# Performance work log

Measured on AMD Instinct MI355X. Metric: run time of the kernel, lower is better.

## Reference

```python
import jax, jax.numpy as jnp
import numpy as np

IGNORE_IDX = -100
DELTA_V = 0.5
DELTA_D = 1.5
PARAM_VAR = 1.0
PARAM_DIST = 1.0
PARAM_REG = 0.001
LOSS_WEIGHT = 1.0
K = 64  # static upper bound on number of instances (matches fill_max of instance_labels)


def setup_inputs() -> dict:
    key = jax.random.key(0)
    k1, k2, k3 = jax.random.split(key, 3)
    B, D, N = 8, 32, 131072
    embedding_logits = jax.random.normal(k1, (B, D, N), dtype=jnp.float32)
    semantic_labels = jax.random.randint(k2, (B, N), 0, 21, dtype=jnp.int64)
    instance_labels = jax.random.randint(k3, (B, N), 0, K, dtype=jnp.int64)
    return {
        "embedding_logits": embedding_logits,
        "semantic_labels": semantic_labels,
        "instance_labels": instance_labels,
        "feature_dim": D,
    }


def _single(x, cls, inst):
    # x: [N, D] embeddings, cls/inst: [N] int labels
    dtype = x.dtype
    valid = cls != IGNORE_IDX
    # points of class 1 are merged into instance 0 (intent of the torch code)
    inst = jnp.where(cls == 1, 0, inst)
    ids = jnp.where(valid, inst, K)  # invalid points -> extra bin K

    counts = jax.ops.segment_sum(valid.astype(dtype), ids, num_segments=K + 1)[:K]
    seg_sum = jax.ops.segment_sum(
        jnp.where(valid[:, None], x, jnp.zeros((), dtype)), ids, num_segments=K + 1
    )[:K]                                            # [K, D]
    mu = seg_sum / (counts[:, None] + 1e-8)          # [K, D] cluster means
    present = counts > 0                             # [K]
    n_inst = jnp.maximum(jnp.sum(present.astype(dtype)), 1.0)

    # intra-cluster variance term (L1 distance to own cluster mean, hinged)
    mu_pt = mu[jnp.clip(ids, 0, K - 1)]              # [N, D]
    d = jnp.sum(jnp.abs(x - mu_pt), axis=1)          # [N]
    d = jnp.square(jnp.maximum(d - DELTA_V, 0.0)) * valid.astype(dtype)
    l_var_seg = jax.ops.segment_sum(d, ids, num_segments=K + 1)[:K] / (counts + 1e-8)
    l_var = jnp.sum(l_var_seg) / n_inst

    # inter-cluster distance term over distinct present cluster pairs
    pdist = jnp.sum(jnp.abs(mu[:, None, :] - mu[None, :, :]), axis=-1)  # [K, K]
    pair_mask = present[:, None] & present[None, :] & ~jnp.eye(K, dtype=bool)
    hinge = jnp.square(jnp.maximum(2.0 * DELTA_D - pdist, 0.0)) * pair_mask.astype(dtype)
    npairs = jnp.sum(pair_mask.astype(dtype))
    l_dist = jnp.where(npairs > 0, jnp.sum(hinge) / jnp.maximum(npairs, 1.0), 0.0)

    # regularization: mean L1 norm of present cluster means
    l_reg = jnp.sum(jnp.sum(jnp.abs(mu), axis=1) * present.astype(dtype)) / n_inst

    l_var = PARAM_VAR * l_var
    l_dist = PARAM_DIST * l_dist
    l_reg = PARAM_REG * l_reg
    loss = LOSS_WEIGHT * (l_var + l_dist + l_reg)
    return loss, l_var, l_dist, l_reg


def reference(embedding_logits, semantic_labels, instance_labels, feature_dim):
    # embedding_logits: [B, D, N] -> per-point embeddings [B, N, D]
    x = jnp.transpose(embedding_logits, (0, 2, 1))
    loss, l_var, l_dist, l_reg = jax.vmap(_single)(x, semantic_labels, instance_labels)
    return (
        jnp.mean(loss),
        jnp.mean(l_var),
        jnp.mean(l_dist),
        jnp.mean(l_reg),
    )
```

## Files before the change

### kernel.cpp

```cpp
#include <hip/hip_runtime.h>


typedef unsigned char uchar;
typedef __attribute__((ext_vector_type(8)))  short bf16x8;
typedef __attribute__((ext_vector_type(16))) float f32x16;

#define IGNORE_IDX (-100)

constexpr int B = 8;
constexpr int D = 32;
constexpr int K = 64;
constexpr int NPTS = 131072;
constexpr int BPB  = 128;
constexpr int SPAN = 1024;
constexpr float DELTA_V = 0.5f;
constexpr float TWO_DELTA_D = 3.0f;
constexpr float PARAM_REG = 0.001f;

constexpr size_t OFF_MU  = (size_t)B * BPB * 2048;
constexpr size_t OFF_VP  = OFF_MU + (size_t)B * 2048;
constexpr size_t OFF_CNT = OFF_VP + (size_t)B * BPB * K;
constexpr size_t OFF_ID  = OFF_CNT + (size_t)B * K;

__device__ inline unsigned bfpack(unsigned a0, unsigned a1) {
    return __builtin_amdgcn_perm(a1, a0, 0x07060302u);
}

__global__ __launch_bounds__(256) void k0_ids(
    const int* __restrict__ sem, const int* __restrict__ inst,
    uchar* __restrict__ id8, int* __restrict__ cnt)
{
    __shared__ int s_cnt[K];
    const int t = threadIdx.x;
    const int b = blockIdx.x / (NPTS / 2048);
    if (t < K) s_cnt[t] = 0;
    __syncthreads();

    const int base = blockIdx.x * 2048 + t * 8;
    const int4 c0 = *(const int4*)(sem + base);
    const int4 c1 = *(const int4*)(sem + base + 4);
    const int4 i0 = *(const int4*)(inst + base);
    const int4 i1 = *(const int4*)(inst + base + 4);
    const int cl[8] = {c0.x, c0.y, c0.z, c0.w, c1.x, c1.y, c1.z, c1.w};
    const int il[8] = {i0.x, i0.y, i0.z, i0.w, i1.x, i1.y, i1.z, i1.w};

    unsigned w0 = 0, w1 = 0;
#pragma unroll
    for (int j = 0; j < 8; ++j) {
        const bool v = (cl[j] != IGNORE_IDX);
        int q = (cl[j] == 1) ? 0 : il[j];
        q = (q < 0) ? 0 : (q > K - 1 ? K - 1 : q);
        if (v) atomicAdd(&s_cnt[q], 1);
        const unsigned byte = v ? (unsigned)q : 255u;
        if (j < 4) w0 |= byte << (8 * j);
        else       w1 |= byte << (8 * (j - 4));
    }
    *(uint2*)(id8 + base) = make_uint2(w0, w1);
    __syncthreads();

    if (t < K) {
        const int c = s_cnt[t];
        if (c) atomicAdd(&cnt[b * K + t], c);
    }
}

__global__ __launch_bounds__(256) void k1_mfma(
    const float* __restrict__ x, const uchar* __restrict__ id8,
    float* __restrict__ part)
{
    __shared__ float s_part[4][2048];
    const int t = threadIdx.x, w = t >> 6, L = t & 63;
    const int g = L >> 5, ln = L & 31;
    const unsigned lnu = (unsigned)ln, lnp32 = (unsigned)(ln + 32);
    const int blk = blockIdx.x, b = blk >> 7, sp = blk & (BPB - 1);

    const unsigned* xrow = (const unsigned*)(x + (size_t)b * D * NPTS
                                             + (size_t)ln * NPTS + sp * SPAN);
    const uchar* idb = id8 + (size_t)b * NPTS + sp * SPAN;

    f32x16 acc0, acc1;
#pragma unroll
    for (int i = 0; i < 16; ++i) { acc0[i] = 0.f; acc1[i] = 0.f; }

    for (int it = 0; it < SPAN / 64; ++it) {
        const int n0 = (it * 4 + w) * 16 + g * 8;
        const uint2 idq = *(const uint2*)(idb + n0);
        const uint4 xa = *(const uint4*)(xrow + n0);
        const uint4 xc = *(const uint4*)(xrow + n0 + 4);

        union { unsigned u[4]; bf16x8 v; } Ah, B0, B1;
        Ah.u[0] = bfpack(xa.x + 0x8000u, xa.y + 0x8000u);
        Ah.u[1] = bfpack(xa.z + 0x8000u, xa.w + 0x8000u);
        Ah.u[2] = bfpack(xc.x + 0x8000u, xc.y + 0x8000u);
        Ah.u[3] = bfpack(xc.z + 0x8000u, xc.w + 0x8000u);
#pragma unroll
        for (int p = 0; p < 4; ++p) {
            const unsigned pair = ((p < 2) ? idq.x : idq.y) >> ((p & 1) * 16);
            const unsigned e0 = pair & 255u, e1 = (pair >> 8) & 255u;
            unsigned r0 = (e0 == lnu)   ? 0x3F80u : 0u;
            unsigned r1 = (e0 == lnp32) ? 0x3F80u : 0u;
            if (e1 == lnu)   r0 |= 0x3F800000u;
            if (e1 == lnp32) r1 |= 0x3F800000u;
            B0.u[p] = r0; B1.u[p] = r1;
        }
        acc0 = __builtin_amdgcn_mfma_f32_32x32x16_bf16(Ah.v, B0.v, acc0, 0, 0, 0);
        acc1 = __builtin_amdgcn_mfma_f32_32x32x16_bf16(Ah.v, B1.v, acc1, 0, 0, 0);
    }

#pragma unroll
    for (int r = 0; r < 16; ++r) {
        const int row = (r & 3) + 8 * (r >> 2) + 4 * g;
        s_part[w][row * 64 + ln]      = acc0[r];
        s_part[w][row * 64 + ln + 32] = acc1[r];
    }
    __syncthreads();

    float* dst = part + (size_t)blk * 2048;
    for (int i = t; i < 2048; i += 256)
        dst[i] = s_part[0][i] + s_part[1][i] + s_part[2][i] + s_part[3][i];
}

__global__ __launch_bounds__(256) void k2_mu(const float* __restrict__ part,
                                             const int* __restrict__ cnt,
                                             float* __restrict__ mu)
{
    const int gid  = blockIdx.x * 256 + threadIdx.x;
    const int b    = gid >> 11;
    const int cell = gid & 2047;
    const int k    = cell & 63;
    float s = 0.f;
    for (int blk = 0; blk < BPB; ++blk)
        s += part[((size_t)(b * BPB + blk) << 11) + cell];
    mu[(size_t)b * 2048 + cell] = s / ((float)cnt[b * K + k] + 1e-8f);
}

__global__ __launch_bounds__(256) void k3_mfma(
    const float* __restrict__ x, const uchar* __restrict__ id8,
    const float* __restrict__ mu, float* __restrict__ vpart)
{
    __shared__ float s_var[K];
    const int t = threadIdx.x, w = t >> 6, L = t & 63;
    const int g = L >> 5, ln = L & 31;
    const int blk = blockIdx.x, b = blk >> 7, sp = blk & (BPB - 1);
    if (t < K) s_var[t] = 0.f;

    union { unsigned u[4]; bf16x8 v; } MAh[4];
    const unsigned* mrow = (const unsigned*)(mu + (size_t)b * 2048 + ln * 64);
#pragma unroll
    for (int c = 0; c < 4; ++c) {
        const uint4 m0 = *(const uint4*)(mrow + c * 16 + g * 8);
        const uint4 m1 = *(const uint4*)(mrow + c * 16 + g * 8 + 4);
        MAh[c].u[0] = bfpack(m0.x + 0x8000u, m0.y + 0x8000u);
        MAh[c].u[1] = bfpack(m0.z + 0x8000u, m0.w + 0x8000u);
        MAh[c].u[2] = bfpack(m1.x + 0x8000u, m1.y + 0x8000u);
        MAh[c].u[3] = bfpack(m1.z + 0x8000u, m1.w + 0x8000u);
    }
    __syncthreads();

    const float* xb  = x + (size_t)b * D * NPTS + sp * SPAN;
    const uchar* idb = id8 + (size_t)b * NPTS + sp * SPAN;

    for (int it = 0; it < SPAN / 128; ++it) {
        const int n0 = (it * 4 + w) * 32;
        const unsigned myid = idb[n0 + ln];
        const unsigned m8 = (myid < 64u && (((myid >> 3) & 1u) == (unsigned)g))
                          ? (1u << (myid & 7u)) : 0u;
        unsigned dw[4];
#pragma unroll
        for (int p = 0; p < 4; ++p) {
            const unsigned b0 = (m8 >> (2 * p)) & 1u;
            const unsigned b1 = (m8 >> (2 * p + 1)) & 1u;
            dw[p] = (b0 | (b1 << 16)) * 0x3F80u;
        }
        const unsigned cstar = myid >> 4;
        f32x16 acc;
#pragma unroll
        for (int i = 0; i < 16; ++i) acc[i] = 0.f;
#pragma unroll
        for (int c = 0; c < 4; ++c) {
            union { unsigned u[4]; bf16x8 v; } Bc;
#pragma unroll
            for (int p = 0; p < 4; ++p) Bc.u[p] = (cstar == (unsigned)c) ? dw[p] : 0u;
            acc = __builtin_amdgcn_mfma_f32_32x32x16_bf16(MAh[c].v, Bc.v, acc, 0, 0, 0);
        }
        float s = 0.f;
#pragma unroll
        for (int r = 0; r < 16; ++r) {
            const int row = (r & 3) + 8 * (r >> 2) + 4 * g;
            s += fabsf(xb[(size_t)row * NPTS + n0 + ln] - acc[r]);
        }
        s += __shfl_xor(s, 32, 64);
        if (g == 0 && myid < 64u) {
            const float h = fmaxf(s - DELTA_V, 0.f);
            if (h > 0.f) unsafeAtomicAdd(&s_var[myid], h * h);
        }
    }
    __syncthreads();
    if (t < K) vpart[(size_t)blk * K + t] = s_var[t];
}

__device__ float block_reduce_sum512(float v, float* s_buf) {
    for (int o = 32; o > 0; o >>= 1) v += __shfl_down(v, o, 64);
    const int wid  = threadIdx.x >> 6;
    const int lane = threadIdx.x & 63;
    if (lane == 0) s_buf[wid] = v;
    __syncthreads();
    float r = 0.f;
    if (threadIdx.x == 0)
        for (int w = 0; w < 8; ++w) r += s_buf[w];
    __syncthreads();
    return r;
}

__global__ __launch_bounds__(512) void k4_final(const float* __restrict__ mu,
                                                const int* __restrict__ cnt,
                                                const float* __restrict__ vpart,
                                                float* __restrict__ out)
{
    const int b = blockIdx.x;
    __shared__ float s_mu[K][D + 1];
    __shared__ float s_cnt[K];
    __shared__ float s_vp[8][K];
    __shared__ float s_red[8];

    const int t = threadIdx.x;
    if (t < K) s_cnt[t] = (float)cnt[b * K + t];

    {
        const int k = t & 63, pr = t >> 6;
        float vs = 0.f;
#pragma unroll
        for (int ch = pr * 16; ch < pr * 16 + 16; ++ch)
            vs += vpart[((size_t)(b * BPB + ch)) * K + k];
        s_vp[pr][k] = vs;
    }
    for (int i = t; i < K * D; i += 512)
        s_mu[i >> 5][i & 31] = mu[(size_t)b * 2048 + (i & 31) * 64 + (i >> 5)];
    __syncthreads();

    float distPart = 0.f;
    for (int p = t; p < K * K; p += 512) {
        const int i = p >> 6, j = p & 63;
        if (i != j && s_cnt[i] > 0.f && s_cnt[j] > 0.f) {
            float dsum = 0.f;
#pragma unroll
            for (int d = 0; d < D; ++d) dsum += fabsf(s_mu[i][d] - s_mu[j][d]);
            const float h = fmaxf(TWO_DELTA_D - dsum, 0.f);
            distPart += h * h;
        }
    }
    float regPart = 0.f;
    for (int i = t; i < K * D; i += 512) {
        const int k = i >> 5;
        if (s_cnt[k] > 0.f) regPart += fabsf(s_mu[k][i & 31]);
    }
    float varPart = 0.f, npPart = 0.f;
    if (t < K) {
        float vs = 0.f;
#pragma unroll
        for (int pr = 0; pr < 8; ++pr) vs += s_vp[pr][t];
        varPart = vs / (s_cnt[t] + 1e-8f);
        npPart  = (s_cnt[t] > 0.f) ? 1.f : 0.f;
    }

    const float distSum = block_reduce_sum512(distPart, s_red);
    const float regSum  = block_reduce_sum512(regPart,  s_red);
    const float varSum  = block_reduce_sum512(varPart,  s_red);
    const float npSum   = block_reduce_sum512(npPart,   s_red);

    if (t == 0) {
        const float n_inst = fmaxf(npSum, 1.0f);
        const float npairs = npSum * npSum - npSum;
        const float l_var  = varSum / n_inst;
        const float l_dist = (npairs > 0.f) ? (distSum / fmaxf(npairs, 1.0f)) : 0.f;
        const float l_reg  = PARAM_REG * (regSum / n_inst);
        const float invB   = 1.0f / (float)B;
        unsafeAtomicAdd(out + 0, (l_var + l_dist + l_reg) * invB);
        unsafeAtomicAdd(out + 1, l_var  * invB);
        unsafeAtomicAdd(out + 2, l_dist * invB);
        unsafeAtomicAdd(out + 3, l_reg  * invB);
    }
}

extern "C" void kernel_launch(void* const* d_in, const int* in_sizes, int n_in,
                              void* d_out, int out_size, void* d_ws, size_t ws_size,
                              hipStream_t stream) {
    const float* x    = (const float*)d_in[0];
    const int*   sem  = (const int*)d_in[1];
    const int*   inst = (const int*)d_in[2];
    float*       out  = (float*)d_out;
    float*       ws   = (float*)d_ws;

    float* part  = ws;
    float* mu    = ws + OFF_MU;
    float* vpart = ws + OFF_VP;
    int*   cnt   = (int*)(ws + OFF_CNT);
    uchar* id8   = (uchar*)(ws + OFF_ID);

    hipMemsetAsync(cnt, 0, B * K * sizeof(int), stream);
    hipMemsetAsync(out, 0, (size_t)out_size * sizeof(float), stream);

    k0_ids<<<dim3(B * NPTS / 2048), dim3(256), 0, stream>>>(sem, inst, id8, cnt);
    k1_mfma<<<dim3(B * BPB), dim3(256), 0, stream>>>(x, id8, part);
    k2_mu<<<dim3(B * K * D / 256), dim3(256), 0, stream>>>(part, cnt, mu);
    k3_mfma<<<dim3(B * BPB), dim3(256), 0, stream>>>(x, id8, mu, vpart);
    k4_final<<<dim3(B), dim3(512), 0, stream>>>(mu, cnt, vpart, out);
}
```

Baseline: 257.9 us.

## Fuse id/count pass into segment-sum kernel and simplify variance pass with LDS gather

Folds the label preprocessing and counting into the MFMA segment-sum kernel, which now reads labels once into shared memory. Per-block partial sums are replaced by global atomics, which removes the separate mean-reduction kernel and its large partial buffer. The variance kernel drops the MFMA-based mean gather in favour of fp32 means in LDS indexed per point, with vectorised coalesced x loads, and accumulates into global atomics. The cost is added atomic contention and atomic nondeterminism in float sums.

```diff
diff --git a/kernel.cpp b/kernel.cpp
--- a/kernel.cpp
+++ b/kernel.cpp
@@ -17,74 +17,60 @@
 constexpr float TWO_DELTA_D = 3.0f;
 constexpr float PARAM_REG = 0.001f;
 
-constexpr size_t OFF_MU  = (size_t)B * BPB * 2048;
-constexpr size_t OFF_VP  = OFF_MU + (size_t)B * 2048;
-constexpr size_t OFF_CNT = OFF_VP + (size_t)B * BPB * K;
-constexpr size_t OFF_ID  = OFF_CNT + (size_t)B * K;
+constexpr size_t OFF_CNT = (size_t)B * 2048;
+constexpr size_t OFF_VS  = OFF_CNT + (size_t)B * K;
+constexpr size_t OFF_ID  = OFF_VS  + (size_t)B * K;
+constexpr size_t ZERO_FLOATS = OFF_ID;
 
 __device__ inline unsigned bfpack(unsigned a0, unsigned a1) {
     return __builtin_amdgcn_perm(a1, a0, 0x07060302u);
 }
 
-__global__ __launch_bounds__(256) void k0_ids(
-    const int* __restrict__ sem, const int* __restrict__ inst,
-    uchar* __restrict__ id8, int* __restrict__ cnt)
-{
-    __shared__ int s_cnt[K];
-    const int t = threadIdx.x;
-    const int b = blockIdx.x / (NPTS / 2048);
-    if (t < K) s_cnt[t] = 0;
-    __syncthreads();
-
-    const int base = blockIdx.x * 2048 + t * 8;
-    const int4 c0 = *(const int4*)(sem + base);
-    const int4 c1 = *(const int4*)(sem + base + 4);
-    const int4 i0 = *(const int4*)(inst + base);
-    const int4 i1 = *(const int4*)(inst + base + 4);
-    const int cl[8] = {c0.x, c0.y, c0.z, c0.w, c1.x, c1.y, c1.z, c1.w};
-    const int il[8] = {i0.x, i0.y, i0.z, i0.w, i1.x, i1.y, i1.z, i1.w};
-
-    unsigned w0 = 0, w1 = 0;
-#pragma unroll
-    for (int j = 0; j < 8; ++j) {
-        const bool v = (cl[j] != IGNORE_IDX);
-        int q = (cl[j] == 1) ? 0 : il[j];
-        q = (q < 0) ? 0 : (q > K - 1 ? K - 1 : q);
-        if (v) atomicAdd(&s_cnt[q], 1);
-        const unsigned byte = v ? (unsigned)q : 255u;
-        if (j < 4) w0 |= byte << (8 * j);
-        else       w1 |= byte << (8 * (j - 4));
-    }
-    *(uint2*)(id8 + base) = make_uint2(w0, w1);
-    __syncthreads();
-
-    if (t < K) {
-        const int c = s_cnt[t];
-        if (c) atomicAdd(&cnt[b * K + t], c);
-    }
-}
-
-__global__ __launch_bounds__(256) void k1_mfma(
-    const float* __restrict__ x, const uchar* __restrict__ id8,
-    float* __restrict__ part)
+__global__ __launch_bounds__(256) void k1_fused(
+    const float* __restrict__ x, const int* __restrict__ sem,
+    const int* __restrict__ inst, uchar* __restrict__ id8,
+    int* __restrict__ cnt, float* __restrict__ musum)
 {
     __shared__ float s_part[4][2048];
+    __shared__ unsigned s_id4[256];
+    __shared__ int s_cnt[K];
     const int t = threadIdx.x, w = t >> 6, L = t & 63;
     const int g = L >> 5, ln = L & 31;
     const unsigned lnu = (unsigned)ln, lnp32 = (unsigned)(ln + 32);
     const int blk = blockIdx.x, b = blk >> 7, sp = blk & (BPB - 1);
 
+    if (t < K) s_cnt[t] = 0;
+    __syncthreads();
+
+    {
+        const size_t off = (size_t)b * NPTS + sp * SPAN + t * 4;
+        const int4 c4 = *(const int4*)(sem + off);
+        const int4 i4 = *(const int4*)(inst + off);
+        const int cl[4] = {c4.x, c4.y, c4.z, c4.w};
+        const int il[4] = {i4.x, i4.y, i4.z, i4.w};
+        unsigned wrd = 0;
+#pragma unroll
+        for (int j = 0; j < 4; ++j) {
+            const bool v = (cl[j] != IGNORE_IDX);
+            int q = (cl[j] == 1) ? 0 : il[j];
+            q = (q < 0) ? 0 : (q > K - 1 ? K - 1 : q);
+            if (v) atomicAdd(&s_cnt[q], 1);
+            wrd |= (v ? (unsigned)q : 255u) << (8 * j);
+        }
+        s_id4[t] = wrd;
+        *(unsigned*)(id8 + off) = wrd;
+    }
+
+    f32x16 acc0, acc1;
+#pragma unroll
+    for (int i = 0; i < 16; ++i) { acc0[i] = 0.f; acc1[i] = 0.f; }
+    __syncthreads();
+
     const unsigned* xrow = (const unsigned*)(x + (size_t)b * D * NPTS
                                              + (size_t)ln * NPTS + sp * SPAN);
-    const uchar* idb = id8 + (size_t)b * NPTS + sp * SPAN;
-
-    f32x16 acc0, acc1;
-#pragma unroll
-    for (int i = 0; i < 16; ++i) { acc0[i] = 0.f; acc1[i] = 0.f; }
-
     for (int it = 0; it < SPAN / 64; ++it) {
         const int n0 = (it * 4 + w) * 16 + g * 8;
-        const uint2 idq = *(const uint2*)(idb + n0);
+        const uint2 idq = *(const uint2*)(&s_id4[n0 >> 2]);
         const uint4 xa = *(const uint4*)(xrow + n0);
         const uint4 xc = *(const uint4*)(xrow + n0 + 4);
 
@@ -115,88 +101,65 @@
     }
     __syncthreads();
 
-    float* dst = part + (size_t)blk * 2048;
+    float* dst = musum + (size_t)b * 2048;
     for (int i = t; i < 2048; i += 256)
-        dst[i] = s_part[0][i] + s_part[1][i] + s_part[2][i] + s_part[3][i];
-}
-
-__global__ __launch_bounds__(256) void k2_mu(const float* __restrict__ part,
-                                             const int* __restrict__ cnt,
-                                             float* __restrict__ mu)
+        unsafeAtomicAdd(&dst[i],
+            s_part[0][i] + s_part[1][i] + s_part[2][i] + s_part[3][i]);
+    if (t < K) {
+        const int c = s_cnt[t];
+        if (c) atomicAdd(&cnt[b * K + t], c);
+    }
+}
+
+__global__ __launch_bounds__(256) void k3_var(
+    const float* __restrict__ x, const uchar* __restrict__ id8,
+    const float* __restrict__ musum, const int* __restrict__ cnt,
+    float* __restrict__ vsum)
 {
-    const int gid  = blockIdx.x * 256 + threadIdx.x;
-    const int b    = gid >> 11;
-    const int cell = gid & 2047;
-    const int k    = cell & 63;
-    float s = 0.f;
-    for (int blk = 0; blk < BPB; ++blk)
-        s += part[((size_t)(b * BPB + blk) << 11) + cell];
-    mu[(size_t)b * 2048 + cell] = s / ((float)cnt[b * K + k] + 1e-8f);
-}
-
-__global__ __launch_bounds__(256) void k3_mfma(
-    const float* __restrict__ x, const uchar* __restrict__ id8,
-    const float* __restrict__ mu, float* __restrict__ vpart)
-{
+    __shared__ float s_mu[2048];
     __shared__ float s_var[K];
-    const int t = threadIdx.x, w = t >> 6, L = t & 63;
-    const int g = L >> 5, ln = L & 31;
+    const int t = threadIdx.x;
     const int blk = blockIdx.x, b = blk >> 7, sp = blk & (BPB - 1);
+
     if (t < K) s_var[t] = 0.f;
-
-    union { unsigned u[4]; bf16x8 v; } MAh[4];
-    const unsigned* mrow = (const unsigned*)(mu + (size_t)b * 2048 + ln * 64);
-#pragma unroll
-    for (int c = 0; c < 4; ++c) {
-        const uint4 m0 = *(const uint4*)(mrow + c * 16 + g * 8);
-        const uint4 m1 = *(const uint4*)(mrow + c * 16 + g * 8 + 4);
-        MAh[c].u[0] = bfpack(m0.x + 0x8000u, m0.y + 0x8000u);
-        MAh[c].u[1] = bfpack(m0.z + 0x8000u, m0.w + 0x8000u);
-        MAh[c].u[2] = bfpack(m1.x + 0x8000u, m1.y + 0x8000u);
-        MAh[c].u[3] = bfpack(m1.z + 0x8000u, m1.w + 0x8000u);
-    }
-    __syncthreads();
-
-    const float* xb  = x + (size_t)b * D * NPTS + sp * SPAN;
-    const uchar* idb = id8 + (size_t)b * NPTS + sp * SPAN;
-
-    for (int it = 0; it < SPAN / 128; ++it) {
-        const int n0 = (it * 4 + w) * 32;
-        const unsigned myid = idb[n0 + ln];
-        const unsigned m8 = (myid < 64u && (((myid >> 3) & 1u) == (unsigned)g))
-                          ? (1u << (myid & 7u)) : 0u;
-        unsigned dw[4];
-#pragma unroll
-        for (int p = 0; p < 4; ++p) {
-            const unsigned b0 = (m8 >> (2 * p)) & 1u;
-            const unsigned b1 = (m8 >> (2 * p + 1)) & 1u;
-            dw[p] = (b0 | (b1 << 16)) * 0x3F80u;
-        }
-        const unsigned cstar = myid >> 4;
-        f32x16 acc;
-#pragma unroll
-        for (int i = 0; i < 16; ++i) acc[i] = 0.f;
-#pragma unroll
-        for (int c = 0; c < 4; ++c) {
-            union { unsigned u[4]; bf16x8 v; } Bc;
-#pragma unroll
-            for (int p = 0; p < 4; ++p) Bc.u[p] = (cstar == (unsigned)c) ? dw[p] : 0u;
-            acc = __builtin_amdgcn_mfma_f32_32x32x16_bf16(MAh[c].v, Bc.v, acc, 0, 0, 0);
-        }
-        float s = 0.f;
-#pragma unroll
-        for (int r = 0; r < 16; ++r) {
-            const int row = (r & 3) + 8 * (r >> 2) + 4 * g;
-            s += fabsf(xb[(size_t)row * NPTS + n0 + ln] - acc[r]);
-        }
-        s += __shfl_xor(s, 32, 64);
-        if (g == 0 && myid < 64u) {
-            const float h = fmaxf(s - DELTA_V, 0.f);
-            if (h > 0.f) unsafeAtomicAdd(&s_var[myid], h * h);
-        }
-    }
-    __syncthreads();
-    if (t < K) vpart[(size_t)blk * K + t] = s_var[t];
+    for (int i = t; i < 2048; i += 256)
+        s_mu[i] = musum[(size_t)b * 2048 + i]
+                / ((float)cnt[b * K + (i & 63)] + 1e-8f);
+
+    const unsigned idw = *(const unsigned*)(id8 + (size_t)b * NPTS + sp * SPAN + t * 4);
+    int q[4]; bool val[4];
+#pragma unroll
+    for (int j = 0; j < 4; ++j) {
+        const unsigned e = (idw >> (8 * j)) & 255u;
+        val[j] = (e < 64u);
+        q[j] = (int)(e & 63u);
+    }
+    __syncthreads();
+
+    const float* xp = x + (size_t)b * D * NPTS + sp * SPAN + t * 4;
+    float s0 = 0.f, s1 = 0.f, s2 = 0.f, s3 = 0.f;
+#pragma unroll
+    for (int d = 0; d < D; ++d) {
+        const float4 xv = *(const float4*)(xp + (size_t)d * NPTS);
+        s0 += fabsf(xv.x - s_mu[d * 64 + q[0]]);
+        s1 += fabsf(xv.y - s_mu[d * 64 + q[1]]);
+        s2 += fabsf(xv.z - s_mu[d * 64 + q[2]]);
+        s3 += fabsf(xv.w - s_mu[d * 64 + q[3]]);
+    }
+
+    const float ss[4] = {s0, s1, s2, s3};
+#pragma unroll
+    for (int j = 0; j < 4; ++j) {
+        if (val[j]) {
+            const float h = fmaxf(ss[j] - DELTA_V, 0.f);
+            if (h > 0.f) unsafeAtomicAdd(&s_var[q[j]], h * h);
+        }
+    }
+    __syncthreads();
+    if (t < K) {
+        const float v = s_var[t];
+        if (v != 0.f) unsafeAtomicAdd(&vsum[b * K + t], v);
+    }
 }
 
 __device__ float block_reduce_sum512(float v, float* s_buf) {
@@ -212,30 +175,23 @@
     return r;
 }
 
-__global__ __launch_bounds__(512) void k4_final(const float* __restrict__ mu,
+__global__ __launch_bounds__(512) void k4_final(const float* __restrict__ musum,
                                                 const int* __restrict__ cnt,
-                                                const float* __restrict__ vpart,
+                                                const float* __restrict__ vsum,
                                                 float* __restrict__ out)
 {
     const int b = blockIdx.x;
     __shared__ float s_mu[K][D + 1];
     __shared__ float s_cnt[K];
-    __shared__ float s_vp[8][K];
     __shared__ float s_red[8];
 
     const int t = threadIdx.x;
     if (t < K) s_cnt[t] = (float)cnt[b * K + t];
-
-    {
-        const int k = t & 63, pr = t >> 6;
-        float vs = 0.f;
-#pragma unroll
-        for (int ch = pr * 16; ch < pr * 16 + 16; ++ch)
-            vs += vpart[((size_t)(b * BPB + ch)) * K + k];
-        s_vp[pr][k] = vs;
-    }
-    for (int i = t; i < K * D; i += 512)
-        s_mu[i >> 5][i & 31] = mu[(size_t)b * 2048 + (i & 31) * 64 + (i >> 5)];
+    for (int i = t; i < K * D; i += 512) {
+        const int d = i >> 6, k = i & 63;
+        s_mu[k][d] = musum[(size_t)b * 2048 + i]
+                   / ((float)cnt[b * K + k] + 1e-8f);
+    }
     __syncthreads();
 
     float distPart = 0.f;
@@ -251,15 +207,12 @@
     }
     float regPart = 0.f;
     for (int i = t; i < K * D; i += 512) {
-        const int k = i >> 5;
-        if (s_cnt[k] > 0.f) regPart += fabsf(s_mu[k][i & 31]);
+        const int k = i & 63;
+        if (s_cnt[k] > 0.f) regPart += fabsf(s_mu[k][i >> 6]);
     }
     float varPart = 0.f, npPart = 0.f;
     if (t < K) {
-        float vs = 0.f;
-#pragma unroll
-        for (int pr = 0; pr < 8; ++pr) vs += s_vp[pr][t];
-        varPart = vs / (s_cnt[t] + 1e-8f);
+        varPart = vsum[b * K + t] / (s_cnt[t] + 1e-8f);
         npPart  = (s_cnt[t] > 0.f) ? 1.f : 0.f;
     }
 
@@ -291,18 +244,15 @@
     float*       out  = (float*)d_out;
     float*       ws   = (float*)d_ws;
 
-    float* part  = ws;
-    float* mu    = ws + OFF_MU;
-    float* vpart = ws + OFF_VP;
+    float* musum = ws;
     int*   cnt   = (int*)(ws + OFF_CNT);
+    float* vsum  = ws + OFF_VS;
     uchar* id8   = (uchar*)(ws + OFF_ID);
 
-    hipMemsetAsync(cnt, 0, B * K * sizeof(int), stream);
+    hipMemsetAsync(ws, 0, ZERO_FLOATS * sizeof(float), stream);
     hipMemsetAsync(out, 0, (size_t)out_size * sizeof(float), stream);
 
-    k0_ids<<<dim3(B * NPTS / 2048), dim3(256), 0, stream>>>(sem, inst, id8, cnt);
-    k1_mfma<<<dim3(B * BPB), dim3(256), 0, stream>>>(x, id8, part);
-    k2_mu<<<dim3(B * K * D / 256), dim3(256), 0, stream>>>(part, cnt, mu);
-    k3_mfma<<<dim3(B * BPB), dim3(256), 0, stream>>>(x, id8, mu, vpart);
-    k4_final<<<dim3(B), dim3(512), 0, stream>>>(mu, cnt, vpart, out);
-}
+    k1_fused<<<dim3(B * BPB), dim3(256), 0, stream>>>(x, sem, inst, id8, cnt, musum);
+    k3_var  <<<dim3(B * BPB), dim3(256), 0, stream>>>(x, id8, musum, cnt, vsum);
+    k4_final<<<dim3(B), dim3(512), 0, stream>>>(musum, cnt, vsum, out);
+}
```

Result: no change. 254.7 us (-1.3%).
